# Kernel tuning notes

Measured on AMD Instinct MI355X. Metric: run time of the kernel, lower is better.

Reference implementation:

```python
import jax, jax.numpy as jnp
import numpy as np

SCALING = 2.0  # alpha / rank = 16 / 8


def _kron(A, B):
    # A: (m, n), B: (p, q) -> (m*p, n*q), same broadcast-multiply-reshape as torch code
    m, n = A.shape
    p, q = B.shape
    return (A[:, None, :, None] * B[None, :, None, :]).reshape(m * p, n * q)


def setup_inputs() -> dict:
    key = jax.random.key(0)
    k1, k2, k3, k4 = jax.random.split(key, 4)
    x = jax.random.normal(k1, (128, 8192), dtype=jnp.float32)
    original_weight = jax.random.normal(k2, (8192, 8192), dtype=jnp.float32) * 0.02
    lokr_A = jax.random.normal(k3, (512, 8192), dtype=jnp.float32) * 0.02
    lokr_B = jax.random.normal(k4, (16, 1), dtype=jnp.float32) * 0.02
    scalar = jnp.ones((1,), dtype=jnp.float32)
    return {"x": x, "original_weight": original_weight, "lokr_A": lokr_A,
            "lokr_B": lokr_B, "scalar": scalar}


def reference(x, original_weight, lokr_A, lokr_B, scalar):
    # delta_W = (A kron B) * scaling ; W_eff = W + scalar * delta_W ; out = x @ W_eff^T
    delta_W = _kron(lokr_A, lokr_B) * SCALING          # (8192, 8192)
    W_eff = original_weight + scalar[0] * delta_W      # bypass_mode with original weight
    return x @ W_eff.T                                 # dropout=0 -> identity
```

## Files before the change

### kernel.cpp

```cpp
#include <hip/hip_runtime.h>


#define M_DIM 128
#define N_DIM 8192
#define K_DIM 8192
#define BN 32
#define BK 64
#define NSTEP (K_DIM / BK)

typedef __attribute__((ext_vector_type(8))) short bf16x8;
typedef __attribute__((ext_vector_type(4))) float f32x4;

__device__ __forceinline__ unsigned short f2bf(float f) {
  unsigned u = __builtin_bit_cast(unsigned, f);
  u += 0x7FFFu + ((u >> 16) & 1u);
  return (unsigned short)(u >> 16);
}

__global__ void convert_x_kernel(const float4* __restrict__ x4,
                                 ushort4* __restrict__ xb4) {
  int t = blockIdx.x * blockDim.x + threadIdx.x;
  const int n4 = M_DIM * K_DIM / 4;
  for (int i = t; i < n4; i += gridDim.x * blockDim.x) {
    float4 v = x4[i];
    ushort4 o;
    o.x = f2bf(v.x); o.y = f2bf(v.y); o.z = f2bf(v.z); o.w = f2bf(v.w);
    xb4[i] = o;
  }
}

#define GLDS2(KOFF, BUF) { \
    __builtin_amdgcn_global_load_lds( \
        (const __attribute__((address_space(1))) unsigned int*)(xs0 + (KOFF)), \
        (__attribute__((address_space(3))) unsigned int*)(&xls[BUF][wv * 1024]), 16, 0, 0); \
    __builtin_amdgcn_global_load_lds( \
        (const __attribute__((address_space(1))) unsigned int*)(xs1 + (KOFF)), \
        (__attribute__((address_space(3))) unsigned int*)(&xls[BUF][wv * 1024 + 512]), 16, 0, 0); \
  }

#define ITER(S, BF, WREG, AREG) { \
    { ushort4 o; o.x = f2bf(WREG.x); o.y = f2bf(WREG.y); \
      o.z = f2bf(WREG.z); o.w = f2bf(WREG.w); \
      *(ushort4*)&wls[BF][t >> 4][(t & 15) * 4] = o; } \
    if (aact) { ushort2 o2; o2.x = f2bf(AREG.x); o2.y = f2bf(AREG.y); \
      *(ushort2*)&wls[BF][32 + (t >> 5)][(t & 31) * 2] = o2; } \
    __syncthreads();   \
    { int kn = ((S) + 2 < NSTEP ? (S) + 2 : NSTEP - 1) * BK; \
      WREG = *(const float4*)(Wp + kn); \
      if (aact) AREG = *(const float2*)(Apt + kn); } \
    { int kx = ((S) + 1 < NSTEP ? (S) + 1 : NSTEP - 1) * BK; \
      GLDS2(kx, (BF) ^ 1); } \
    _Pragma("unroll") \
    for (int kk = 0; kk < 2; ++kk) { \
      bf16x8 xf = *(const bf16x8*)&xls[BF][(wv * 16 + l15) * BK + (((kk * 4 + l4) ^ (l15 & 7)) * 8)]; \
      bf16x8 w0 = *(const bf16x8*)&wls[BF][l15][kk * 32 + l4 * 8]; \
      bf16x8 w1 = *(const bf16x8*)&wls[BF][16 + l15][kk * 32 + l4 * 8]; \
      bf16x8 af = *(const bf16x8*)&wls[BF][32 + (l15 >> 3)][kk * 32 + l4 * 8]; \
      accW0 = __builtin_amdgcn_mfma_f32_16x16x32_bf16(xf, w0, accW0, 0, 0, 0); \
      accW1 = __builtin_amdgcn_mfma_f32_16x16x32_bf16(xf, w1, accW1, 0, 0, 0); \
      accY  = __builtin_amdgcn_mfma_f32_16x16x32_bf16(xf, af, accY, 0, 0, 0); \
    } \
  }

__global__ __launch_bounds__(512) void lokr_main(
    const float* __restrict__ W,
    const float* __restrict__ A,
    const float* __restrict__ Bv,
    const float* __restrict__ scal,
    const unsigned short* __restrict__ xb,
    float* __restrict__ out)
{
  __shared__ unsigned short xls[2][M_DIM * BK];
  __shared__ unsigned short wls[2][34][72];

  const int t    = threadIdx.x;
  const int lane = t & 63;
  const int wv   = t >> 6;
  const int b    = blockIdx.x;
  const int l15  = lane & 15;
  const int l4   = lane >> 4;

  const float sB = 2.0f * scal[0] * Bv[l15];

  const float* Wp  = W + (size_t)(b * BN + (t >> 4)) * K_DIM + (t & 15) * 4;
  const bool  aact = (t < 64);
  const float* Apt = A + (size_t)(2 * b + ((t >> 5) & 1)) * K_DIM + (t & 31) * 2;

  const int xr0 = wv * 16 + (lane >> 3);
  const int xr1 = xr0 + 8;
  const int xc  = lane & 7;
  const unsigned short* xs0 = xb + (size_t)xr0 * K_DIM + ((xc ^ (xr0 & 7)) * 8);
  const unsigned short* xs1 = xb + (size_t)xr1 * K_DIM + ((xc ^ (xr1 & 7)) * 8);

  f32x4 accW0 = {0.f, 0.f, 0.f, 0.f};
  f32x4 accW1 = {0.f, 0.f, 0.f, 0.f};
  f32x4 accY  = {0.f, 0.f, 0.f, 0.f};

  float4 wA = *(const float4*)(Wp);
  float4 wB = *(const float4*)(Wp + BK);
  float2 aA = {0.f, 0.f}, aB = {0.f, 0.f};
  if (aact) { aA = *(const float2*)(Apt); aB = *(const float2*)(Apt + BK); }
  GLDS2(0, 0);

  for (int s2 = 0; s2 < NSTEP; s2 += 2) {
    ITER(s2,     0, wA, aA);
    ITER(s2 + 1, 1, wB, aB);
  }

  const size_t ob = (size_t)(wv * 16 + l4 * 4) * N_DIM + (size_t)b * BN + l15;
#pragma unroll
  for (int nf = 0; nf < 2; ++nf) {
    f32x4 aw = nf ? accW1 : accW0;
#pragma unroll
    for (int r = 0; r < 4; ++r) {
      float y2v = __shfl(accY[r], (lane & 48) | (nf << 3), 64);
      out[ob + (size_t)r * N_DIM + nf * 16] = aw[r] + sB * y2v;
    }
  }
}

extern "C" void kernel_launch(void* const* d_in, const int* in_sizes, int n_in,
                              void* d_out, int out_size, void* d_ws, size_t ws_size,
                              hipStream_t stream) {
  const float* x    = (const float*)d_in[0];
  const float* W    = (const float*)d_in[1];
  const float* A    = (const float*)d_in[2];
  const float* Bv   = (const float*)d_in[3];
  const float* scal = (const float*)d_in[4];
  float* out = (float*)d_out;

  unsigned short* xb = (unsigned short*)d_ws;

  convert_x_kernel<<<512, 256, 0, stream>>>((const float4*)x, (ushort4*)xb);
  lokr_main<<<N_DIM / BN, 512, 0, stream>>>(W, A, Bv, scal, xb, out);
}
```

Before: 448.7 us.

## Software-pipeline W/A loads with inline asm and explicit vmcnt waits

Replaces the compiler-generated W and A global loads with inline-asm loads and explicit s_waitcnt vmcnt counters. The bf16 conversion and LDS store of the next tile now happen after the MFMAs of the current step, so global-load latency overlaps compute without waiting for all outstanding loads. All waves now issue the A loads (only wave 0 converts them), and the barrier is a raw s_barrier preceded by an lgkmcnt wait. The hand-counted vmcnt values are fragile and can race if the compiler reorders or adds memory ops.

```diff
diff --git a/kernel.cpp b/kernel.cpp
--- a/kernel.cpp
+++ b/kernel.cpp
@@ -29,6 +29,14 @@
   }
 }
 
+#define GLW(dst, p) asm volatile("global_load_dwordx4 %0, %1, off" \
+                                 : "=&v"(dst) : "v"(p) : "memory")
+#define GLA(dst, p) asm volatile("global_load_dwordx2 %0, %1, off" \
+                                 : "=&v"(dst) : "v"(p) : "memory")
+#define WAITV(n) { asm volatile("s_waitcnt vmcnt(" #n ")" ::: "memory"); \
+                   __builtin_amdgcn_sched_barrier(0); }
+#define WAITL0   asm volatile("s_waitcnt lgkmcnt(0)" ::: "memory")
+
 #define GLDS2(KOFF, BUF) { \
     __builtin_amdgcn_global_load_lds( \
         (const __attribute__((address_space(1))) unsigned int*)(xs0 + (KOFF)), \
@@ -38,18 +46,24 @@
         (__attribute__((address_space(3))) unsigned int*)(&xls[BUF][wv * 1024 + 512]), 16, 0, 0); \
   }
 
-#define ITER(S, BF, WREG, AREG) { \
-    { ushort4 o; o.x = f2bf(WREG.x); o.y = f2bf(WREG.y); \
-      o.z = f2bf(WREG.z); o.w = f2bf(WREG.w); \
-      *(ushort4*)&wls[BF][t >> 4][(t & 15) * 4] = o; } \
-    if (aact) { ushort2 o2; o2.x = f2bf(AREG.x); o2.y = f2bf(AREG.y); \
-      *(ushort2*)&wls[BF][32 + (t >> 5)][(t & 31) * 2] = o2; } \
-    __syncthreads();   \
-    { int kn = ((S) + 2 < NSTEP ? (S) + 2 : NSTEP - 1) * BK; \
-      WREG = *(const float4*)(Wp + kn); \
-      if (aact) AREG = *(const float2*)(Apt + kn); } \
+#define CONVW(BFW, WREG) { ushort4 o; \
+    o.x = f2bf(WREG.x); o.y = f2bf(WREG.y); \
+    o.z = f2bf(WREG.z); o.w = f2bf(WREG.w); \
+    *(ushort4*)&wls[BFW][t >> 4][(t & 15) * 4] = o; }
+
+#define CONVA(BFW, AREG) if (wv == 0) { ushort2 o2; \
+    o2.x = f2bf(AREG.x); o2.y = f2bf(AREG.y); \
+    *(ushort2*)&wls[BFW][32 + (lane >> 5)][(lane & 31) * 2] = o2; }
+
+#define ITER(S, BF, WCUR, ACUR, WNEW, ANEW) { \
+    WAITL0; \
+    __builtin_amdgcn_s_barrier(); \
     { int kx = ((S) + 1 < NSTEP ? (S) + 1 : NSTEP - 1) * BK; \
       GLDS2(kx, (BF) ^ 1); } \
+    { int kn = ((S) + 2 < NSTEP ? (S) + 2 : NSTEP - 1) * BK; \
+      GLW(WNEW, Wp + kn); \
+      GLA(ANEW, Apt + kn); } \
+    WAITV(6);   \
     _Pragma("unroll") \
     for (int kk = 0; kk < 2; ++kk) { \
       bf16x8 xf = *(const bf16x8*)&xls[BF][(wv * 16 + l15) * BK + (((kk * 4 + l4) ^ (l15 & 7)) * 8)]; \
@@ -60,6 +74,9 @@
       accW1 = __builtin_amdgcn_mfma_f32_16x16x32_bf16(xf, w1, accW1, 0, 0, 0); \
       accY  = __builtin_amdgcn_mfma_f32_16x16x32_bf16(xf, af, accY, 0, 0, 0); \
     } \
+    WAITV(4);   \
+    CONVW((BF) ^ 1, WCUR); \
+    CONVA((BF) ^ 1, ACUR); \
   }
 
 __global__ __launch_bounds__(512) void lokr_main(
@@ -83,8 +100,7 @@
   const float sB = 2.0f * scal[0] * Bv[l15];
 
   const float* Wp  = W + (size_t)(b * BN + (t >> 4)) * K_DIM + (t & 15) * 4;
-  const bool  aact = (t < 64);
-  const float* Apt = A + (size_t)(2 * b + ((t >> 5) & 1)) * K_DIM + (t & 31) * 2;
+  const float* Apt = A + (size_t)(2 * b + (lane >> 5)) * K_DIM + (lane & 31) * 2;
 
   const int xr0 = wv * 16 + (lane >> 3);
   const int xr1 = xr0 + 8;
@@ -96,15 +112,20 @@
   f32x4 accW1 = {0.f, 0.f, 0.f, 0.f};
   f32x4 accY  = {0.f, 0.f, 0.f, 0.f};
 
-  float4 wA = *(const float4*)(Wp);
-  float4 wB = *(const float4*)(Wp + BK);
-  float2 aA = {0.f, 0.f}, aB = {0.f, 0.f};
-  if (aact) { aA = *(const float2*)(Apt); aB = *(const float2*)(Apt + BK); }
+  float4 wA, wB;
+  float2 aA, aB;
+  GLW(wA, Wp);
+  GLA(aA, Apt);
+  WAITV(0);
+  CONVW(0, wA);
+  CONVA(0, aA);
   GLDS2(0, 0);
+  GLW(wA, Wp + BK);
+  GLA(aA, Apt + BK);
 
   for (int s2 = 0; s2 < NSTEP; s2 += 2) {
-    ITER(s2,     0, wA, aA);
-    ITER(s2 + 1, 1, wB, aB);
+    ITER(s2,     0, wA, aA, wB, aB);
+    ITER(s2 + 1, 1, wB, aB, wA, aA);
   }
 
   const size_t ob = (size_t)(wv * 16 + l4 * 4) * N_DIM + (size_t)b * BN + l15;
```

After: 450.9 us. About the same (+0.5%).
